# Kernel optimization log

Hardware: AMD Instinct MI355X
Metric: run time of the kernel (lower is better)

## Reference

```python
import jax, jax.numpy as jnp
import numpy as np

STRIDE = 4
WH, WW = 16, 16
NUM_LEVELS = 3


def setup_inputs() -> dict:
    key = jax.random.key(0)
    x = jax.random.normal(key, (16, 256, 64, 64), dtype=jnp.float32)
    return {"x": x}


def reference(x):
    bs, c, h, w = x.shape
    out_h = (h - WH) // STRIDE + 1
    out_w = (w - WW) // STRIDE + 1
    parts = []
    for lvl in range(NUM_LEVELS):
        k = WH // (2 ** lvl)           # sub-pool kernel (torch: h // 2**i on the window)
        n_h = WH // k                  # sub-cells per window, height
        n_w = WW // k                  # sub-cells per window, width
        # stride-1 k x k max pool over the full image; window cell (i,j,p,q)
        # equals pooled[i*STRIDE + p*k, j*STRIDE + q*k]
        pooled = jax.lax.reduce_window(
            x, -jnp.inf, jax.lax.max,
            (1, 1, k, k), (1, 1, 1, 1), 'VALID')  # [bs,c,h-k+1,w-k+1]
        rows = (jnp.arange(out_h) * STRIDE)[:, None] + (jnp.arange(n_h) * k)[None, :]
        cols = (jnp.arange(out_w) * STRIDE)[:, None] + (jnp.arange(n_w) * k)[None, :]
        g = pooled[:, :, rows.reshape(-1), :][:, :, :, cols.reshape(-1)]
        # [bs,c,out_h*n_h,out_w*n_w] -> [bs, c*n_h*n_w, out_h, out_w]
        g = g.reshape(bs, c, out_h, n_h, out_w, n_w)
        g = g.transpose(0, 1, 3, 5, 2, 4).reshape(bs, c * n_h * n_w, out_h, out_w)
        parts.append(g)
    # torch concatenates level outputs along the flattened feature dim per window
    return jnp.concatenate(parts, axis=1)
```

## Files before the change

### kernel.cpp

```cpp
#include <hip/hip_runtime.h>


#define BS 16
#define CH 256
#define H 64
#define W 64
#define OUT_H 13
#define OUT_W 13
#define OUT_C 5376
#define OHW (OUT_H * OUT_W)

__global__ __launch_bounds__(256) void spp_kernel(const float* __restrict__ x,
                                                  float* __restrict__ out) {
    const int plane = blockIdx.x;
    const int b = plane >> 8;
    const int c = plane & 255;
    const int t = threadIdx.x;

    __shared__ float rowmax[64][17];
    __shared__ float m4s[16][17];
    __shared__ float m8s[15][16];
    __shared__ float m16s[13][14];

    const float* xp = x + (size_t)plane * (H * W);

#pragma unroll
    for (int it = 0; it < 4; ++it) {
        int idx = t + it * 256;
        int row = idx >> 4;
        int c4 = idx & 15;
        float4 v = reinterpret_cast<const float4*>(xp)[idx];
        rowmax[row][c4] = fmaxf(fmaxf(v.x, v.y), fmaxf(v.z, v.w));
    }
    __syncthreads();

    {
        int a = t >> 4, bb = t & 15;
        float m = rowmax[4 * a][bb];
        m = fmaxf(m, rowmax[4 * a + 1][bb]);
        m = fmaxf(m, rowmax[4 * a + 2][bb]);
        m = fmaxf(m, rowmax[4 * a + 3][bb]);
        m4s[a][bb] = m;
    }
    __syncthreads();

    if (t < 225) {
        int a = t / 15, bb = t % 15;
        m8s[a][bb] = fmaxf(fmaxf(m4s[a][bb], m4s[a + 1][bb]),
                           fmaxf(m4s[a][bb + 1], m4s[a + 1][bb + 1]));
    }
    __syncthreads();

    if (t < 169) {
        int i = t / 13, j = t % 13;
        m16s[i][j] = fmaxf(fmaxf(m8s[i][j], m8s[i + 2][j]),
                           fmaxf(m8s[i][j + 2], m8s[i + 2][j + 2]));
    }
    __syncthreads();

    if (t < OHW) {
        const int i = t / 13, j = t % 13;
        float* outb = out + (size_t)b * (OUT_C * OHW);

        outb[(size_t)c * OHW + t] = m16s[i][j];

        float* o1 = outb + (size_t)(256 + c * 4) * OHW;
#pragma unroll
        for (int p = 0; p < 2; ++p)
#pragma unroll
            for (int q = 0; q < 2; ++q)
                o1[(p * 2 + q) * OHW + t] = m8s[i + 2 * p][j + 2 * q];

        float* o2 = outb + (size_t)(1280 + c * 16) * OHW;
#pragma unroll
        for (int p = 0; p < 4; ++p)
#pragma unroll
            for (int q = 0; q < 4; ++q)
                o2[(p * 4 + q) * OHW + t] = m4s[i + p][j + q];
    }
}

extern "C" void kernel_launch(void* const* d_in, const int* in_sizes, int n_in,
                              void* d_out, int out_size, void* d_ws, size_t ws_size,
                              hipStream_t stream) {
    const float* x = (const float*)d_in[0];
    float* out = (float*)d_out;
    spp_kernel<<<dim3(BS * CH), dim3(256), 0, stream>>>(x, out);
}
```

Before: 24.22 us.

## Stage SPP outputs in shared memory and write them with vectorized float4 stores

Each thread now computes its 4x4 block max straight from four float4 global loads, which drops the rowmax shared-memory stage and one barrier. The 16x16 level is computed in the output phase instead of in a separate pass. All three levels are written to shared-memory staging buffers and then copied to global memory as contiguous float4 stores instead of scalar strided stores. The aim is better store efficiency and fewer synchronisations, at the cost of more shared memory per block and a different global load pattern.

```diff
diff --git a/kernel.cpp b/kernel.cpp
--- a/kernel.cpp
+++ b/kernel.cpp
@@ -3,8 +3,6 @@
 
 #define BS 16
 #define CH 256
-#define H 64
-#define W 64
 #define OUT_H 13
 #define OUT_W 13
 #define OUT_C 5376
@@ -17,66 +15,63 @@
     const int c = plane & 255;
     const int t = threadIdx.x;
 
-    __shared__ float rowmax[64][17];
     __shared__ float m4s[16][17];
     __shared__ float m8s[15][16];
-    __shared__ float m16s[13][14];
+    __shared__ alignas(16) float out0s[OHW];
+    __shared__ alignas(16) float out1s[4 * OHW];
+    __shared__ alignas(16) float out2s[16 * OHW];
 
-    const float* xp = x + (size_t)plane * (H * W);
-
-#pragma unroll
-    for (int it = 0; it < 4; ++it) {
-        int idx = t + it * 256;
-        int row = idx >> 4;
-        int c4 = idx & 15;
-        float4 v = reinterpret_cast<const float4*>(xp)[idx];
-        rowmax[row][c4] = fmaxf(fmaxf(v.x, v.y), fmaxf(v.z, v.w));
-    }
-    __syncthreads();
+    const float* xp = x + (size_t)plane * 4096;
 
     {
-        int a = t >> 4, bb = t & 15;
-        float m = rowmax[4 * a][bb];
-        m = fmaxf(m, rowmax[4 * a + 1][bb]);
-        m = fmaxf(m, rowmax[4 * a + 2][bb]);
-        m = fmaxf(m, rowmax[4 * a + 3][bb]);
-        m4s[a][bb] = m;
+        const int a = t >> 4, bb = t & 15;
+        const float* base = xp + a * 256 + bb * 4;
+        float4 v0 = *reinterpret_cast<const float4*>(base);
+        float4 v1 = *reinterpret_cast<const float4*>(base + 64);
+        float4 v2 = *reinterpret_cast<const float4*>(base + 128);
+        float4 v3 = *reinterpret_cast<const float4*>(base + 192);
+        float m01 = fmaxf(fmaxf(fmaxf(v0.x, v0.y), fmaxf(v0.z, v0.w)),
+                          fmaxf(fmaxf(v1.x, v1.y), fmaxf(v1.z, v1.w)));
+        float m23 = fmaxf(fmaxf(fmaxf(v2.x, v2.y), fmaxf(v2.z, v2.w)),
+                          fmaxf(fmaxf(v3.x, v3.y), fmaxf(v3.z, v3.w)));
+        m4s[a][bb] = fmaxf(m01, m23);
     }
     __syncthreads();
 
     if (t < 225) {
-        int a = t / 15, bb = t % 15;
-        m8s[a][bb] = fmaxf(fmaxf(m4s[a][bb], m4s[a + 1][bb]),
-                           fmaxf(m4s[a][bb + 1], m4s[a + 1][bb + 1]));
-    }
-    __syncthreads();
-
-    if (t < 169) {
-        int i = t / 13, j = t % 13;
-        m16s[i][j] = fmaxf(fmaxf(m8s[i][j], m8s[i + 2][j]),
-                           fmaxf(m8s[i][j + 2], m8s[i + 2][j + 2]));
+        int i = t / 15, j = t % 15;
+        m8s[i][j] = fmaxf(fmaxf(m4s[i][j], m4s[i + 1][j]),
+                          fmaxf(m4s[i][j + 1], m4s[i + 1][j + 1]));
     }
     __syncthreads();
 
     if (t < OHW) {
         const int i = t / 13, j = t % 13;
-        float* outb = out + (size_t)b * (OUT_C * OHW);
-
-        outb[(size_t)c * OHW + t] = m16s[i][j];
-
-        float* o1 = outb + (size_t)(256 + c * 4) * OHW;
+        out0s[t] = fmaxf(fmaxf(m8s[i][j], m8s[i + 2][j]),
+                         fmaxf(m8s[i][j + 2], m8s[i + 2][j + 2]));
 #pragma unroll
         for (int p = 0; p < 2; ++p)
 #pragma unroll
             for (int q = 0; q < 2; ++q)
-                o1[(p * 2 + q) * OHW + t] = m8s[i + 2 * p][j + 2 * q];
-
-        float* o2 = outb + (size_t)(1280 + c * 16) * OHW;
+                out1s[(p * 2 + q) * OHW + t] = m8s[i + 2 * p][j + 2 * q];
 #pragma unroll
         for (int p = 0; p < 4; ++p)
 #pragma unroll
             for (int q = 0; q < 4; ++q)
-                o2[(p * 4 + q) * OHW + t] = m4s[i + p][j + q];
+                out2s[(p * 4 + q) * OHW + t] = m4s[i + p][j + q];
+    }
+    __syncthreads();
+
+    float* outb = out + (size_t)b * (OUT_C * OHW);
+    float4* o2v = reinterpret_cast<float4*>(outb + (size_t)(1280 + c * 16) * OHW);
+    const float4* s2v = reinterpret_cast<const float4*>(out2s);
+#pragma unroll
+    for (int k = t; k < 4 * OHW; k += 256)
+        o2v[k] = s2v[k];
+    if (t < OHW) {
+        float4* o1v = reinterpret_cast<float4*>(outb + (size_t)(256 + c * 4) * OHW);
+        o1v[t] = reinterpret_cast<const float4*>(out1s)[t];
+        outb[(size_t)c * OHW + t] = out0s[t];
     }
 }
 
```

Result: no change. 24.16 us (-0.2%).
